# Optimization experiments

Hardware: AMD Instinct MI355X
Metric: run time of the kernel (lower is better)

The kernel has to match this reference:

```python
import math
import jax, jax.numpy as jnp
import numpy as np

B, S, D, H, DFF, BASE = 2, 2048, 1024, 16, 4096, 10000.0
HD = D // H  # 64


def setup_inputs() -> dict:
    key = jax.random.key(0)
    ks = jax.random.split(key, 16)
    sc = 0.02
    inp = {
        "x": jax.random.normal(ks[0], (B, S, D), jnp.float32),
        "positions": jnp.arange(S, dtype=jnp.int32),
        "wq": jax.random.normal(ks[1], (D, D), jnp.float32) * sc,
        "bq": jnp.zeros((D,), jnp.float32),
        "wk": jax.random.normal(ks[2], (D, D), jnp.float32) * sc,
        "bk": jnp.zeros((D,), jnp.float32),
        "wv": jax.random.normal(ks[3], (D, D), jnp.float32) * sc,
        "bv": jnp.zeros((D,), jnp.float32),
        "wo": jax.random.normal(ks[4], (D, D), jnp.float32) * sc,
        "bo": jnp.zeros((D,), jnp.float32),
        "phase_bias": jax.random.uniform(ks[5], (H, HD), jnp.float32, -2.0 * math.pi, 0.0),
        "w1": jax.random.normal(ks[6], (D, DFF), jnp.float32) * sc,
        "b1": jnp.zeros((DFF,), jnp.float32),
        "w2": jax.random.normal(ks[7], (DFF, D), jnp.float32) * sc,
        "b2": jnp.zeros((D,), jnp.float32),
        "g1": jnp.ones((D,), jnp.float32),
        "be1": jnp.zeros((D,), jnp.float32),
        "g2": jnp.ones((D,), jnp.float32),
        "be2": jnp.zeros((D,), jnp.float32),
    }
    return inp


def _layernorm(x, g, b):
    mu = jnp.mean(x, -1, keepdims=True)
    var = jnp.mean(jnp.square(x - mu), -1, keepdims=True)
    return (x - mu) / jnp.sqrt(var + 1e-5) * g + b


def _block(x, positions, wq, bq, wk, bk, wv, bv, wo, bo, phase_bias,
           w1, b1, w2, b2, g1, be1, g2, be2):
    # projections -> (B, H, S, HD)
    def heads(w, b):
        return (x @ w + b).reshape(B, S, H, HD).transpose(0, 2, 1, 3)
    q, k, v = heads(wq, bq), heads(wk, bk), heads(wv, bv)

    # PoPE: magnitudes via softplus, phases from position*freq (+ clamped bias for k)
    mu_q = jax.nn.softplus(q)
    mu_k = jax.nn.softplus(k)
    freqs = 1.0 / BASE ** (jnp.arange(HD, dtype=jnp.float32) / HD)      # (HD,)
    pos_ph = positions[:, None].astype(jnp.float32) * freqs[None, :]     # (S, HD)
    q_ph = pos_ph[None, None]                                            # (1,1,S,HD)
    cb = jnp.clip(phase_bias, -2.0 * math.pi, 0.0)
    k_ph = pos_ph[None, None] + cb[None, :, None, :]                     # (1,H,S,HD)
    q_p = jnp.concatenate([mu_q * jnp.cos(q_ph), mu_q * jnp.sin(q_ph)], -1)  # (B,H,S,2HD)
    k_p = jnp.concatenate([mu_k * jnp.cos(k_ph), mu_k * jnp.sin(k_ph)], -1)

    # manual attention with causal mask and softmax1
    scale = 1.0 / math.sqrt(2 * HD)
    scores = jnp.einsum("bhqd,bhkd->bhqk", q_p, k_p) * scale
    causal = jnp.triu(jnp.ones((S, S), bool), 1)
    scores = jnp.where(causal, -jnp.inf, scores)
    m = jnp.max(scores, -1, keepdims=True)  # finite: diagonal always unmasked
    e = jnp.exp(scores - m)
    w = e / (jnp.exp(-m) + jnp.sum(e, -1, keepdims=True))
    attn = jnp.einsum("bhqk,bhkd->bhqd", w, v)
    attn = attn.transpose(0, 2, 1, 3).reshape(B, S, D) @ wo + bo

    h = _layernorm(x + attn, g1, be1)
    ff = jax.nn.relu(h @ w1 + b1) @ w2 + b2
    return _layernorm(h + ff, g2, be2)


def reference(x, positions, wq, bq, wk, bk, wv, bv, wo, bo, phase_bias,
              w1, b1, w2, b2, g1, be1, g2, be2):
    return _block(x, positions, wq, bq, wk, bk, wv, bv, wo, bo, phase_bias,
                  w1, b1, w2, b2, g1, be1, g2, be2)
```

## Files before the change

### kernel.cpp

```cpp
#include <hip/hip_runtime.h>
#include <hip/hip_bf16.h>
#include <math.h>

#define NB 2
#define NS 2048
#define ND 1024
#define NH 16
#define NHD 64
#define NDFF 4096

typedef __attribute__((ext_vector_type(4))) float f32x4;
typedef __attribute__((ext_vector_type(8))) short bf16x8;

__device__ __forceinline__ short f2bf(float f) {
  union { float f; unsigned u; } v; v.f = f;
  unsigned r = v.u + 0x7fffu + ((v.u >> 16) & 1u);
  return (short)(r >> 16);
}
__device__ __forceinline__ float bf2f(unsigned short u) {
  union { unsigned u; float f; } v; v.u = ((unsigned)u) << 16; return v.f;
}
__device__ __forceinline__ float softplus_f(float x) {
  return fmaxf(x, 0.f) + log1pf(__expf(-fabsf(x)));
}
__device__ __forceinline__ void gl16(const short* g, short* l) {
  __builtin_amdgcn_global_load_lds(
      (const __attribute__((address_space(1))) void*)g,
      (__attribute__((address_space(3))) void*)l, 16, 0, 0);
}

__global__ __launch_bounds__(256) void k_wt(const float* __restrict__ W,
    short* __restrict__ Wt, int K, int N) {
  __shared__ float t[64][65];
  const int k0 = blockIdx.y * 64, n0 = blockIdx.x * 64;
  for (int i = threadIdx.x; i < 4096; i += 256) {
    const int r = i >> 6, c = i & 63;
    t[r][c] = W[(size_t)(k0 + r) * N + n0 + c];
  }
  __syncthreads();
  for (int i = threadIdx.x; i < 4096; i += 256) {
    const int r = i >> 6, c = i & 63;
    Wt[(size_t)(n0 + r) * K + k0 + c] = f2bf(t[c][r]);
  }
}

__global__ __launch_bounds__(256) void k_xb(const float* __restrict__ x,
    short* __restrict__ xb, int n8) {
  const int i = blockIdx.x * 256 + threadIdx.x;
  if (i >= n8) return;
  const float4 a = ((const float4*)x)[i * 2];
  const float4 b = ((const float4*)x)[i * 2 + 1];
  short tmp[8] = { f2bf(a.x), f2bf(a.y), f2bf(a.z), f2bf(a.w),
                   f2bf(b.x), f2bf(b.y), f2bf(b.z), f2bf(b.w) };
  *(int4*)&xb[(size_t)i * 8] = *(const int4*)tmp;
}

__global__ __launch_bounds__(256) void k_prep_v(const short* __restrict__ vb,
    short* __restrict__ vt) {
  __shared__ short t[64][72];
  const int bh = blockIdx.y, b = bh >> 4, h = bh & 15;
  const int s0 = blockIdx.x * 64;
  for (int i = threadIdx.x; i < 512; i += 256) {
    const int sl = i >> 3, d8 = (i & 7) * 8;
    int4 vv = *(const int4*)&vb[((size_t)(b * NS + s0 + sl) * NH + h) * NHD + d8];
    const short* sp = (const short*)&vv;
#pragma unroll
    for (int j = 0; j < 8; j++) t[d8 + j][sl] = sp[j];
  }
  __syncthreads();
  for (int i = threadIdx.x; i < 512; i += 256) {
    const int d = i >> 3, c8 = (i & 7) * 8;
    *(int4*)&vt[((size_t)bh * 64 + d) * NS + s0 + c8] = *(const int4*)&t[d][c8];
  }
}

__global__ __launch_bounds__(256) void k_pope(const short* __restrict__ qb,
    const short* __restrict__ kb, const int* __restrict__ positions,
    const float* __restrict__ phb, short* __restrict__ qp,
    short* __restrict__ kp) {
  const size_t i8 = ((size_t)blockIdx.x * 256 + threadIdx.x) * 8;
  const int d0 = (int)(i8 & 63);
  const int h  = (int)((i8 >> 6) & 15);
  const int s  = (int)((i8 >> 10) & 2047);
  const int b  = (int)(i8 >> 21);
  const float posf = (float)positions[s];
  int4 qv = *(const int4*)&qb[i8];
  int4 kv = *(const int4*)&kb[i8];
  const short* qs = (const short*)&qv;
  const short* ks = (const short*)&kv;
  short qc[8], qsn[8], kc[8], ksn[8];
#pragma unroll
  for (int j = 0; j < 8; j++) {
    const int d = d0 + j;
    const float freq = __expf(-(float)d * (float)(9.210340371976184 / 64.0));
    const float muq = softplus_f(bf2f((unsigned short)qs[j]));
    const float muk = softplus_f(bf2f((unsigned short)ks[j]));
    float cb = phb[h * 64 + d];
    cb = fminf(fmaxf(cb, -6.283185307179586f), 0.f);
    float snq, csq, snk, csk;
    __sincosf(posf * freq, &snq, &csq);
    __sincosf(posf * freq + cb, &snk, &csk);
    qc[j] = f2bf(muq * csq); qsn[j] = f2bf(muq * snq);
    kc[j] = f2bf(muk * csk); ksn[j] = f2bf(muk * snk);
  }
  const size_t o = (((size_t)(b * 16 + h) * NS + s) * 128) + d0;
  *(int4*)&qp[o] = *(const int4*)qc;
  *(int4*)&qp[o + 64] = *(const int4*)qsn;
  *(int4*)&kp[o] = *(const int4*)kc;
  *(int4*)&kp[o + 64] = *(const int4*)ksn;
}

#define BKK 32

__device__ __forceinline__ void gemm_core(const short* __restrict__ A,
    const short* __restrict__ Wt, const int K, const int kbeg, const int kend,
    const int row0, const int col0, short* lsA, short* lsB, f32x4 acc[4][4]) {
  const int tid = threadIdx.x;
  const int lane = tid & 63, wave = tid >> 6;
  const int lr = lane & 15, lk8 = (lane >> 4) << 3;
  const int wr = wave >> 1, wc = wave & 1;
  const int srow = lane >> 2, scol = (lane & 3) << 3;
  const int wbase = wave * 32;
#pragma unroll
  for (int m = 0; m < 4; m++)
#pragma unroll
    for (int n = 0; n < 4; n++) acc[m][n] = 0.f;
  const short* gA0 = &A[(size_t)(row0 + wbase + srow) * K + scol];
  const short* gA1 = gA0 + (size_t)16 * K;
  const short* gB0 = &Wt[(size_t)(col0 + wbase + srow) * K + scol];
  const short* gB1 = gB0 + (size_t)16 * K;
  short* const lA0 = lsA + wbase * 32;
  short* const lB0 = lsB + wbase * 32;
  auto stage = [&](int buf, int kk) {
    const int o = buf * 4096;
    gl16(gA0 + kk, lA0 + o);
    gl16(gA1 + kk, lA0 + o + 512);
    gl16(gB0 + kk, lB0 + o);
    gl16(gB1 + kk, lB0 + o + 512);
  };
  stage(0, kbeg);
  __syncthreads();
  int cur = 0;
  for (int k0 = kbeg; k0 < kend; k0 += BKK) {
    if (k0 + BKK < kend) stage(cur ^ 1, k0 + BKK);
    const short* la = lsA + cur * 4096;
    const short* lb = lsB + cur * 4096;
    bf16x8 af[4], bf_[4];
#pragma unroll
    for (int m = 0; m < 4; m++)
      af[m] = *(const bf16x8*)&la[(wr * 64 + m * 16 + lr) * 32 + lk8];
#pragma unroll
    for (int n = 0; n < 4; n++)
      bf_[n] = *(const bf16x8*)&lb[(wc * 64 + n * 16 + lr) * 32 + lk8];
#pragma unroll
    for (int m = 0; m < 4; m++)
#pragma unroll
      for (int n = 0; n < 4; n++)
        acc[m][n] = __builtin_amdgcn_mfma_f32_16x16x32_bf16(af[m], bf_[n], acc[m][n], 0, 0, 0);
    __syncthreads();
    cur ^= 1;
  }
}

template<int RELU, int OUTBF16>
__global__ __launch_bounds__(256) void k_gemm(const short* __restrict__ A,
    const short* __restrict__ Wt, const float* __restrict__ bias,
    void* __restrict__ C, int M, int N, int K) {
  __shared__ short lsA[2 * 4096], lsB[2 * 4096];
  f32x4 acc[4][4];
  const int row0 = blockIdx.y * 128, col0 = blockIdx.x * 128;
  gemm_core(A, Wt, K, 0, K, row0, col0, lsA, lsB, acc);
  const int lane = threadIdx.x & 63, wave = threadIdx.x >> 6;
  const int lr = lane & 15, r4 = (lane >> 4) << 2;
  const int wr = wave >> 1, wc = wave & 1;
#pragma unroll
  for (int m = 0; m < 4; m++) {
#pragma unroll
    for (int n = 0; n < 4; n++) {
      const int col = col0 + wc * 64 + n * 16 + lr;
      const float bv = bias[col];
#pragma unroll
      for (int r = 0; r < 4; r++) {
        const int row = row0 + wr * 64 + m * 16 + r4 + r;
        float val = acc[m][n][r] + bv;
        if (RELU) val = fmaxf(val, 0.f);
        if (OUTBF16) ((short*)C)[(size_t)row * N + col] = f2bf(val);
        else ((float*)C)[(size_t)row * N + col] = val;
      }
    }
  }
}

__global__ __launch_bounds__(256) void k_gemm3(const short* __restrict__ xb,
    const short* __restrict__ wqT, const short* __restrict__ wkT,
    const short* __restrict__ wvT, const float* __restrict__ bq,
    const float* __restrict__ bk, const float* __restrict__ bv,
    short* __restrict__ qb, short* __restrict__ kb, short* __restrict__ vb) {
  __shared__ short lsA[2 * 4096], lsB[2 * 4096];
  const int z = blockIdx.z;
  const short* Wt = (z == 0) ? wqT : (z == 1) ? wkT : wvT;
  const float* bias = (z == 0) ? bq : (z == 1) ? bk : bv;
  short* C = (z == 0) ? qb : (z == 1) ? kb : vb;
  f32x4 acc[4][4];
  const int row0 = blockIdx.y * 128, col0 = blockIdx.x * 128;
  gemm_core(xb, Wt, ND, 0, ND, row0, col0, lsA, lsB, acc);
  const int lane = threadIdx.x & 63, wave = threadIdx.x >> 6;
  const int lr = lane & 15, r4 = (lane >> 4) << 2;
  const int wr = wave >> 1, wc = wave & 1;
#pragma unroll
  for (int m = 0; m < 4; m++) {
#pragma unroll
    for (int n = 0; n < 4; n++) {
      const int col = col0 + wc * 64 + n * 16 + lr;
      const float bvs = bias[col];
#pragma unroll
      for (int r = 0; r < 4; r++) {
        const int row = row0 + wr * 64 + m * 16 + r4 + r;
        C[(size_t)row * ND + col] = f2bf(acc[m][n][r] + bvs);
      }
    }
  }
}

__global__ __launch_bounds__(256) void k_gemm_sk(const short* __restrict__ A,
    const short* __restrict__ Wt, float* __restrict__ C0, float* __restrict__ C1,
    int M, int N, int K) {
  __shared__ short lsA[2 * 4096], lsB[2 * 4096];
  f32x4 acc[4][4];
  const int z = blockIdx.z;
  const int khalf = K >> 1, kbeg = z * khalf, kend = kbeg + khalf;
  const int row0 = blockIdx.y * 128, col0 = blockIdx.x * 128;
  gemm_core(A, Wt, K, kbeg, kend, row0, col0, lsA, lsB, acc);
  float* C = z ? C1 : C0;
  const int lane = threadIdx.x & 63, wave = threadIdx.x >> 6;
  const int lr = lane & 15, r4 = (lane >> 4) << 2;
  const int wr = wave >> 1, wc = wave & 1;
#pragma unroll
  for (int m = 0; m < 4; m++) {
#pragma unroll
    for (int n = 0; n < 4; n++) {
      const int col = col0 + wc * 64 + n * 16 + lr;
#pragma unroll
      for (int r = 0; r < 4; r++) {
        const int row = row0 + wr * 64 + m * 16 + r4 + r;
        C[(size_t)row * N + col] = acc[m][n][r];
      }
    }
  }
}

__device__ __forceinline__ void attn_proc(bf16x8 aq[4], f32x4 acc_o[4],
    float m_r[4], float l_r[4], const int rowb, const int kb,
    const short (*kpl)[136], const short (*vl)[72], short (*pl)[72],
    const int lr, const int lk) {
  f32x4 s_acc[4];
#pragma unroll
  for (int n = 0; n < 4; n++) s_acc[n] = 0.f;
#pragma unroll
  for (int ks = 0; ks < 4; ks++) {
    bf16x8 bk_[4];
#pragma unroll
    for (int n = 0; n < 4; n++)
      bk_[n] = *(const bf16x8*)&kpl[n * 16 + lr][ks * 32 + lk * 8];
#pragma unroll
    for (int n = 0; n < 4; n++)
      s_acc[n] = __builtin_amdgcn_mfma_f32_16x16x32_bf16(aq[ks], bk_[n], s_acc[n], 0, 0, 0);
  }
  const float scale = 0.08838834764831845f;
  float pmax[4];
#pragma unroll
  for (int r = 0; r < 4; r++) pmax[r] = -INFINITY;
#pragma unroll
  for (int n = 0; n < 4; n++) {
#pragma unroll
    for (int r = 0; r < 4; r++) {
      const int rel = rowb + lk * 4 + r - kb;
      float sv = s_acc[n][r] * scale;
      sv = (n * 16 + lr <= rel) ? sv : -INFINITY;
      s_acc[n][r] = sv;
      pmax[r] = fmaxf(pmax[r], sv);
    }
  }
#pragma unroll
  for (int off = 8; off; off >>= 1)
#pragma unroll
    for (int r = 0; r < 4; r++) pmax[r] = fmaxf(pmax[r], __shfl_xor(pmax[r], off));
  float fac[4], rs[4];
#pragma unroll
  for (int r = 0; r < 4; r++) {
    const float nm = fmaxf(m_r[r], pmax[r]);
    fac[r] = __expf(m_r[r] - nm);
    m_r[r] = nm;
    rs[r] = 0.f;
  }
#pragma unroll
  for (int n = 0; n < 4; n++) {
#pragma unroll
    for (int r = 0; r < 4; r++) {
      const float p = __expf(s_acc[n][r] - m_r[r]);
      s_acc[n][r] = p;
      rs[r] += p;
    }
  }
#pragma unroll
  for (int off = 8; off; off >>= 1)
#pragma unroll
    for (int r = 0; r < 4; r++) rs[r] += __shfl_xor(rs[r], off);
#pragma unroll
  for (int r = 0; r < 4; r++) l_r[r] = l_r[r] * fac[r] + rs[r];
#pragma unroll
  for (int n = 0; n < 4; n++)
#pragma unroll
    for (int r = 0; r < 4; r++)
      pl[lk * 4 + r][n * 16 + lr] = f2bf(s_acc[n][r]);
#pragma unroll
  for (int n = 0; n < 4; n++)
#pragma unroll
    for (int r = 0; r < 4; r++) acc_o[n][r] *= fac[r];
#pragma unroll
  for (int ks = 0; ks < 2; ks++) {
    const bf16x8 ap = *(const bf16x8*)&pl[lr][ks * 32 + lk * 8];
    bf16x8 bv_[4];
#pragma unroll
    for (int nd = 0; nd < 4; nd++)
      bv_[nd] = *(const bf16x8*)&vl[nd * 16 + lr][ks * 32 + lk * 8];
#pragma unroll
    for (int nd = 0; nd < 4; nd++)
      acc_o[nd] = __builtin_amdgcn_mfma_f32_16x16x32_bf16(ap, bv_[nd], acc_o[nd], 0, 0, 0);
  }
}

__global__ __launch_bounds__(512) void k_attn2(
    const short* __restrict__ qp, const short* __restrict__ kp,
    const short* __restrict__ vt, short* __restrict__ attn) {
  __shared__ short kp_l[2][64][136];
  __shared__ short v_l[2][64][72];
  __shared__ short p_l[8][16][72];
  const int bh = blockIdx.y, b = bh >> 4, h = bh & 15;
  const int tL = blockIdx.x, tH = 15 - tL;
  const int q0L = tL * 128, q0H = tH * 128;
  const int tid = threadIdx.x, wave = tid >> 6, lane = tid & 63;
  const int lr = lane & 15, lk = lane >> 4;

  bf16x8 aqH[4], aqL[4];
  {
    const short* qrH = qp + ((size_t)bh * NS + q0H + wave * 16 + lr) * 128;
    const short* qrL = qp + ((size_t)bh * NS + q0L + wave * 16 + lr) * 128;
#pragma unroll
    for (int ks = 0; ks < 4; ks++) {
      aqH[ks] = *(const bf16x8*)&qrH[ks * 32 + lk * 8];
      aqL[ks] = *(const bf16x8*)&qrL[ks * 32 + lk * 8];
    }
  }
  f32x4 accH[4], accL[4];
  float mH[4], lH[4], mL[4], lL[4];
#pragma unroll
  for (int r = 0; r < 4; r++) { mH[r] = -INFINITY; lH[r] = 0.f; mL[r] = -INFINITY; lL[r] = 0.f; }
#pragma unroll
  for (int n = 0; n < 4; n++) { accH[n] = 0.f; accL[n] = 0.f; }

  const short* kpb = kp + (size_t)bh * NS * 128;
  const short* vtb = vt + (size_t)bh * 64 * NS;
  const int nch = q0H / 64 + 2;
  const int rowbH = q0H + wave * 16, rowbL = q0L + wave * 16;

  const int krow = tid >> 3, kcol = (tid & 7) * 16;
  const int vrow = tid >> 3, vcol = (tid & 7) * 8;

  int4 rk0, rk1, rv;
  {
    const short* s = &kpb[(size_t)krow * 128 + kcol];
    rk0 = ((const int4*)s)[0]; rk1 = ((const int4*)s)[1];
    rv = *(const int4*)&vtb[(size_t)vrow * NS + vcol];
  }
  ((int4*)&kp_l[0][krow][kcol])[0] = rk0;
  ((int4*)&kp_l[0][krow][kcol])[1] = rk1;
  *(int4*)&v_l[0][vrow][vcol] = rv;
  __syncthreads();

  for (int c = 0; c < nch; c++) {
    const int kb = c * 64;
    const int cur = c & 1;
    const bool more = (c + 1) < nch;
    if (more) {
      const int kb2 = kb + 64;
      const short* s = &kpb[(size_t)(kb2 + krow) * 128 + kcol];
      rk0 = ((const int4*)s)[0]; rk1 = ((const int4*)s)[1];
      rv = *(const int4*)&vtb[(size_t)vrow * NS + kb2 + vcol];
    }
    if (rowbH + 15 >= kb)
      attn_proc(aqH, accH, mH, lH, rowbH, kb, kp_l[cur], v_l[cur], p_l[wave], lr, lk);
    if (rowbL + 15 >= kb)
      attn_proc(aqL, accL, mL, lL, rowbL, kb, kp_l[cur], v_l[cur], p_l[wave], lr, lk);
    __syncthreads();
    if (more) {
      ((int4*)&kp_l[cur ^ 1][krow][kcol])[0] = rk0;
      ((int4*)&kp_l[cur ^ 1][krow][kcol])[1] = rk1;
      *(int4*)&v_l[cur ^ 1][vrow][vcol] = rv;
    }
    __syncthreads();
  }
#pragma unroll
  for (int r = 0; r < 4; r++) {
    lH[r] = 1.f / (__expf(-mH[r]) + lH[r]);
    lL[r] = 1.f / (__expf(-mL[r]) + lL[r]);
  }
#pragma unroll
  for (int nd = 0; nd < 4; nd++) {
#pragma unroll
    for (int r = 0; r < 4; r++) {
      const int d = nd * 16 + lr;
      const int rowH = q0H + wave * 16 + lk * 4 + r;
      const int rowL = q0L + wave * 16 + lk * 4 + r;
      attn[(((size_t)b * NS + rowH) * NH + h) * NHD + d] = f2bf(accH[nd][r] * lH[r]);
      attn[(((size_t)b * NS + rowL) * NH + h) * NHD + d] = f2bf(accL[nd][r] * lL[r]);
    }
  }
}

template<int RBF16, int OUTBF16>
__global__ __launch_bounds__(256) void k_ln3(const float* __restrict__ A0,
    const float* __restrict__ A1, const float* __restrict__ badd,
    const void* __restrict__ Rv, const float* __restrict__ g,
    const float* __restrict__ be, void* __restrict__ out) {
  const int row = blockIdx.x, tid = threadIdx.x;
  const float4 a0 = ((const float4*)(A0 + (size_t)row * ND))[tid];
  const float4 a1 = ((const float4*)(A1 + (size_t)row * ND))[tid];
  const float4 bd = ((const float4*)badd)[tid];
  float r0, r1, r2, r3;
  if (RBF16) {
    short4 rr = *(const short4*)((const short*)Rv + (size_t)row * ND + tid * 4);
    r0 = bf2f((unsigned short)rr.x); r1 = bf2f((unsigned short)rr.y);
    r2 = bf2f((unsigned short)rr.z); r3 = bf2f((unsigned short)rr.w);
  } else {
    const float4 rr = ((const float4*)((const float*)Rv + (size_t)row * ND))[tid];
    r0 = rr.x; r1 = rr.y; r2 = rr.z; r3 = rr.w;
  }
  const float x0 = a0.x + a1.x + bd.x + r0;
  const float x1 = a0.y + a1.y + bd.y + r1;
  const float x2 = a0.z + a1.z + bd.z + r2;
  const float x3 = a0.w + a1.w + bd.w + r3;
  float s = x0 + x1 + x2 + x3;
  float sq = x0 * x0 + x1 * x1 + x2 * x2 + x3 * x3;
#pragma unroll
  for (int off = 32; off; off >>= 1) {
    s += __shfl_xor(s, off);
    sq += __shfl_xor(sq, off);
  }
  __shared__ float ss[4], ssq[4];
  const int wave = tid >> 6, lane = tid & 63;
  if (lane == 0) { ss[wave] = s; ssq[wave] = sq; }
  __syncthreads();
  s = ss[0] + ss[1] + ss[2] + ss[3];
  sq = ssq[0] + ssq[1] + ssq[2] + ssq[3];
  const float mu = s * (1.f / (float)ND);
  const float var = sq * (1.f / (float)ND) - mu * mu;
  const float rstd = rsqrtf(var + 1e-5f);
  const float4 gg = ((const float4*)g)[tid];
  const float4 bb = ((const float4*)be)[tid];
  const float o0 = (x0 - mu) * rstd * gg.x + bb.x;
  const float o1 = (x1 - mu) * rstd * gg.y + bb.y;
  const float o2 = (x2 - mu) * rstd * gg.z + bb.z;
  const float o3 = (x3 - mu) * rstd * gg.w + bb.w;
  if (OUTBF16) {
    short4 ov = { f2bf(o0), f2bf(o1), f2bf(o2), f2bf(o3) };
    *(short4*)((short*)out + (size_t)row * ND + tid * 4) = ov;
  } else {
    float4 ov = { o0, o1, o2, o3 };
    ((float4*)((float*)out + (size_t)row * ND))[tid] = ov;
  }
}

extern "C" void kernel_launch(void* const* d_in, const int* in_sizes, int n_in,
                              void* d_out, int out_size, void* d_ws, size_t ws_size,
                              hipStream_t stream) {
  const float* x   = (const float*)d_in[0];
  const int*   pos = (const int*)d_in[1];
  const float* wq  = (const float*)d_in[2];
  const float* bq  = (const float*)d_in[3];
  const float* wk  = (const float*)d_in[4];
  const float* bk  = (const float*)d_in[5];
  const float* wv  = (const float*)d_in[6];
  const float* bv  = (const float*)d_in[7];
  const float* wo  = (const float*)d_in[8];
  const float* bo  = (const float*)d_in[9];
  const float* phb = (const float*)d_in[10];
  const float* w1  = (const float*)d_in[11];
  const float* b1  = (const float*)d_in[12];
  const float* w2  = (const float*)d_in[13];
  const float* b2  = (const float*)d_in[14];
  const float* g1  = (const float*)d_in[15];
  const float* be1 = (const float*)d_in[16];
  const float* g2  = (const float*)d_in[17];
  const float* be2 = (const float*)d_in[18];

  char* ws = (char*)d_ws;
  const size_t MB = 1024 * 1024;
  if (ws_size < 112 * MB) return;
  short* qb     = (short*)(ws + 0 * MB);
  short* kb     = (short*)(ws + 8 * MB);
  short* vb     = (short*)(ws + 16 * MB);
  short* qp     = (short*)(ws + 24 * MB);
  short* kp     = (short*)(ws + 40 * MB);
  short* vt     = (short*)(ws + 56 * MB);
  short* xb     = (short*)(ws + 64 * MB);
  short* attnb  = (short*)(ws + 72 * MB);
  float* attnC0 = (float*)(ws + 0 * MB);
  float* attnC1 = (float*)(ws + 24 * MB);
  short* hb     = (short*)(ws + 16 * MB);
  short* ffh    = (short*)(ws + 40 * MB);
  float* ffC0   = (float*)(ws + 72 * MB);
  float* ffC1   = (float*)(ws + 0 * MB);
  short* wqT    = (short*)(ws + 88 * MB);
  short* wkT    = (short*)(ws + 90 * MB);
  short* wvT    = (short*)(ws + 92 * MB);
  short* woT    = (short*)(ws + 94 * MB);
  short* w1T    = (short*)(ws + 96 * MB);
  short* w2T    = (short*)(ws + 104 * MB);

  dim3 blk(256);
  k_wt<<<dim3(16, 16), blk, 0, stream>>>(wq, wqT, ND, ND);
  k_wt<<<dim3(16, 16), blk, 0, stream>>>(wk, wkT, ND, ND);
  k_wt<<<dim3(16, 16), blk, 0, stream>>>(wv, wvT, ND, ND);
  k_wt<<<dim3(16, 16), blk, 0, stream>>>(wo, woT, ND, ND);
  k_wt<<<dim3(64, 16), blk, 0, stream>>>(w1, w1T, ND, NDFF);
  k_wt<<<dim3(16, 64), blk, 0, stream>>>(w2, w2T, NDFF, ND);
  k_xb<<<dim3((NB * NS * ND / 8 + 255) / 256), blk, 0, stream>>>(x, xb, NB * NS * ND / 8);
  k_gemm3<<<dim3(ND / 128, (NB * NS) / 128, 3), blk, 0, stream>>>(
      xb, wqT, wkT, wvT, bq, bk, bv, qb, kb, vb);
  k_pope<<<dim3(NB * NS * ND / 8 / 256), blk, 0, stream>>>(qb, kb, pos, phb, qp, kp);
  k_prep_v<<<dim3(NS / 64, NB * NH), blk, 0, stream>>>(vb, vt);
  k_attn2<<<dim3(8, NB * NH), dim3(512), 0, stream>>>(qp, kp, vt, attnb);
  k_gemm_sk<<<dim3(ND / 128, (NB * NS) / 128, 2), blk, 0, stream>>>(
      attnb, woT, attnC0, attnC1, NB * NS, ND, ND);
  k_ln3<0, 1><<<dim3(NB * NS), blk, 0, stream>>>(attnC0, attnC1, bo, x, g1, be1, hb);
  k_gemm<1, 1><<<dim3(NDFF / 128, (NB * NS) / 128), blk, 0, stream>>>(
      hb, w1T, b1, ffh, NB * NS, NDFF, ND);
  k_gemm_sk<<<dim3(ND / 128, (NB * NS) / 128, 2), blk, 0, stream>>>(
      ffh, w2T, ffC0, ffC1, NB * NS, ND, NDFF);
  k_ln3<1, 0><<<dim3(NB * NS), blk, 0, stream>>>(ffC0, ffC1, b2, hb, g2, be2, (float*)d_out);
}
```

Before: 322.8 us.

## Drop online max in softmax1 attention and remap GEMM tiles across XCDs

Attention no longer tracks a running max. Softmax1 is evaluated as exp(s)/(1+sum exp(s)) directly, which removes the per-chunk max shuffles, rescale factors and accumulator rescaling. The causal mask is applied only on diagonal chunks, the row-sum reduction is deferred to the end, and one __syncthreads per chunk is removed. Separately, the GEMM kernels remap block indices so each XCD handles a contiguous group of row tiles, aiming for better L2 reuse. Without the max subtraction, exp can overflow if scores grow large (near 88), so this depends on scores staying bounded.

```diff
diff --git a/kernel.cpp b/kernel.cpp
--- a/kernel.cpp
+++ b/kernel.cpp
@@ -27,6 +27,14 @@
   __builtin_amdgcn_global_load_lds(
       (const __attribute__((address_space(1))) void*)g,
       (__attribute__((address_space(3))) void*)l, 16, 0, 0);
+}
+__device__ __forceinline__ void xcd_map(int& row0, int& col0) {
+  const int gx = gridDim.x, gy = gridDim.y;
+  const int bid = blockIdx.y * gx + blockIdx.x;
+  const int rows_px = gy >> 3;
+  const int xcd = bid & 7, l = bid >> 3;
+  row0 = (xcd * rows_px + (l % rows_px)) * 128;
+  col0 = (l / rows_px) * 128;
 }
 
 __global__ __launch_bounds__(256) void k_wt(const float* __restrict__ W,
@@ -168,7 +176,8 @@
     void* __restrict__ C, int M, int N, int K) {
   __shared__ short lsA[2 * 4096], lsB[2 * 4096];
   f32x4 acc[4][4];
-  const int row0 = blockIdx.y * 128, col0 = blockIdx.x * 128;
+  int row0, col0;
+  xcd_map(row0, col0);
   gemm_core(A, Wt, K, 0, K, row0, col0, lsA, lsB, acc);
   const int lane = threadIdx.x & 63, wave = threadIdx.x >> 6;
   const int lr = lane & 15, r4 = (lane >> 4) << 2;
@@ -202,7 +211,8 @@
   const float* bias = (z == 0) ? bq : (z == 1) ? bk : bv;
   short* C = (z == 0) ? qb : (z == 1) ? kb : vb;
   f32x4 acc[4][4];
-  const int row0 = blockIdx.y * 128, col0 = blockIdx.x * 128;
+  int row0, col0;
+  xcd_map(row0, col0);
   gemm_core(xb, Wt, ND, 0, ND, row0, col0, lsA, lsB, acc);
   const int lane = threadIdx.x & 63, wave = threadIdx.x >> 6;
   const int lr = lane & 15, r4 = (lane >> 4) << 2;
@@ -229,7 +239,8 @@
   f32x4 acc[4][4];
   const int z = blockIdx.z;
   const int khalf = K >> 1, kbeg = z * khalf, kend = kbeg + khalf;
-  const int row0 = blockIdx.y * 128, col0 = blockIdx.x * 128;
+  int row0, col0;
+  xcd_map(row0, col0);
   gemm_core(A, Wt, K, kbeg, kend, row0, col0, lsA, lsB, acc);
   float* C = z ? C1 : C0;
   const int lane = threadIdx.x & 63, wave = threadIdx.x >> 6;
@@ -249,8 +260,8 @@
   }
 }
 
-__device__ __forceinline__ void attn_proc(bf16x8 aq[4], f32x4 acc_o[4],
-    float m_r[4], float l_r[4], const int rowb, const int kb,
+__device__ __forceinline__ void attn_proc(const bf16x8 aq[4], f32x4 acc_o[4],
+    float l_p[4], const int rowb, const int kb,
     const short (*kpl)[136], const short (*vl)[72], short (*pl)[72],
     const int lr, const int lk) {
   f32x4 s_acc[4];
@@ -267,56 +278,28 @@
       s_acc[n] = __builtin_amdgcn_mfma_f32_16x16x32_bf16(aq[ks], bk_[n], s_acc[n], 0, 0, 0);
   }
   const float scale = 0.08838834764831845f;
-  float pmax[4];
-#pragma unroll
-  for (int r = 0; r < 4; r++) pmax[r] = -INFINITY;
+  const bool domask = (kb + 63 > rowb);
 #pragma unroll
   for (int n = 0; n < 4; n++) {
 #pragma unroll
     for (int r = 0; r < 4; r++) {
-      const int rel = rowb + lk * 4 + r - kb;
-      float sv = s_acc[n][r] * scale;
-      sv = (n * 16 + lr <= rel) ? sv : -INFINITY;
-      s_acc[n][r] = sv;
-      pmax[r] = fmaxf(pmax[r], sv);
-    }
-  }
-#pragma unroll
-  for (int off = 8; off; off >>= 1)
-#pragma unroll
-    for (int r = 0; r < 4; r++) pmax[r] = fmaxf(pmax[r], __shfl_xor(pmax[r], off));
-  float fac[4], rs[4];
-#pragma unroll
-  for (int r = 0; r < 4; r++) {
-    const float nm = fmaxf(m_r[r], pmax[r]);
-    fac[r] = __expf(m_r[r] - nm);
-    m_r[r] = nm;
-    rs[r] = 0.f;
-  }
-#pragma unroll
-  for (int n = 0; n < 4; n++) {
-#pragma unroll
-    for (int r = 0; r < 4; r++) {
-      const float p = __expf(s_acc[n][r] - m_r[r]);
+      const float sv = s_acc[n][r] * scale;
+      float p;
+      if (domask) {
+        const int rel = rowb + lk * 4 + r - kb;
+        p = (n * 16 + lr <= rel) ? __expf(sv) : 0.f;
+      } else {
+        p = __expf(sv);
+      }
       s_acc[n][r] = p;
-      rs[r] += p;
-    }
-  }
-#pragma unroll
-  for (int off = 8; off; off >>= 1)
-#pragma unroll
-    for (int r = 0; r < 4; r++) rs[r] += __shfl_xor(rs[r], off);
-#pragma unroll
-  for (int r = 0; r < 4; r++) l_r[r] = l_r[r] * fac[r] + rs[r];
+      l_p[r] += p;
+    }
+  }
 #pragma unroll
   for (int n = 0; n < 4; n++)
 #pragma unroll
     for (int r = 0; r < 4; r++)
       pl[lk * 4 + r][n * 16 + lr] = f2bf(s_acc[n][r]);
-#pragma unroll
-  for (int n = 0; n < 4; n++)
-#pragma unroll
-    for (int r = 0; r < 4; r++) acc_o[n][r] *= fac[r];
 #pragma unroll
   for (int ks = 0; ks < 2; ks++) {
     const bf16x8 ap = *(const bf16x8*)&pl[lr][ks * 32 + lk * 8];
@@ -353,9 +336,9 @@
     }
   }
   f32x4 accH[4], accL[4];
-  float mH[4], lH[4], mL[4], lL[4];
-#pragma unroll
-  for (int r = 0; r < 4; r++) { mH[r] = -INFINITY; lH[r] = 0.f; mL[r] = -INFINITY; lL[r] = 0.f; }
+  float lH[4], lL[4];
+#pragma unroll
+  for (int r = 0; r < 4; r++) { lH[r] = 0.f; lL[r] = 0.f; }
 #pragma unroll
   for (int n = 0; n < 4; n++) { accH[n] = 0.f; accL[n] = 0.f; }
 
@@ -389,10 +372,9 @@
       rv = *(const int4*)&vtb[(size_t)vrow * NS + kb2 + vcol];
     }
     if (rowbH + 15 >= kb)
-      attn_proc(aqH, accH, mH, lH, rowbH, kb, kp_l[cur], v_l[cur], p_l[wave], lr, lk);
+      attn_proc(aqH, accH, lH, rowbH, kb, kp_l[cur], v_l[cur], p_l[wave], lr, lk);
     if (rowbL + 15 >= kb)
-      attn_proc(aqL, accL, mL, lL, rowbL, kb, kp_l[cur], v_l[cur], p_l[wave], lr, lk);
-    __syncthreads();
+      attn_proc(aqL, accL, lL, rowbL, kb, kp_l[cur], v_l[cur], p_l[wave], lr, lk);
     if (more) {
       ((int4*)&kp_l[cur ^ 1][krow][kcol])[0] = rk0;
       ((int4*)&kp_l[cur ^ 1][krow][kcol])[1] = rk1;
@@ -402,8 +384,14 @@
   }
 #pragma unroll
   for (int r = 0; r < 4; r++) {
-    lH[r] = 1.f / (__expf(-mH[r]) + lH[r]);
-    lL[r] = 1.f / (__expf(-mL[r]) + lL[r]);
+    float sH = lH[r], sL = lL[r];
+#pragma unroll
+    for (int off = 8; off; off >>= 1) {
+      sH += __shfl_xor(sH, off);
+      sL += __shfl_xor(sL, off);
+    }
+    lH[r] = 1.f / (1.f + sH);
+    lL[r] = 1.f / (1.f + sL);
   }
 #pragma unroll
   for (int nd = 0; nd < 4; nd++) {
```

New measurement: 295.6 us. -8.4%, faster.
